# Kernel tuning notes

Hardware: AMD Instinct MI355X
Metric: run time of the kernel (lower is better)

## Reference

```python
import jax, jax.numpy as jnp
import numpy as np

B, S, D, H = 2, 2048, 1024, 16
HD = D // H  # head_dim = 64
INIT_STD = 0.02


def rotate_half(x):
    half = x.shape[-1] // 2
    return jnp.concatenate((-x[..., half:], x[..., :half]), axis=-1)


def setup_inputs() -> dict:
    key = jax.random.key(0)
    ks = jax.random.split(key, 6)
    inputs_q = jax.random.normal(ks[0], (B, S, D), dtype=jnp.float32)
    # causal mask, shape [B, 1, S, S] (broadcasts over heads)
    mask = jnp.broadcast_to(jnp.tril(jnp.ones((S, S), dtype=bool))[None, None], (B, 1, S, S))
    Wq = jax.random.normal(ks[1], (D, D), dtype=jnp.float32) * INIT_STD
    Wk = jax.random.normal(ks[2], (D, D), dtype=jnp.float32) * INIT_STD
    Wv = jax.random.normal(ks[3], (D, D), dtype=jnp.float32) * INIT_STD
    Wo = jax.random.normal(ks[4], (D, D), dtype=jnp.float32) * INIT_STD
    bq = jnp.zeros((D,), jnp.float32)
    bk = jnp.zeros((D,), jnp.float32)
    bv = jnp.zeros((D,), jnp.float32)
    bo = jnp.zeros((D,), jnp.float32)
    return {"inputs_q": inputs_q, "mask": mask, "Wq": Wq, "bq": bq, "Wk": Wk, "bk": bk,
            "Wv": Wv, "bv": bv, "Wo": Wo, "bo": bo}


def reference(inputs_q, mask, Wq, bq, Wk, bk, Wv, bv, Wo, bo):
    b, s, d = inputs_q.shape
    h, hd = H, d // H
    # QKV projections, split heads -> [b, s, h, hd]
    q = (inputs_q @ Wq + bq).reshape(b, s, h, hd)
    k = (inputs_q @ Wk + bk).reshape(b, s, h, hd)
    v = (inputs_q @ Wv + bv).reshape(b, s, h, hd)
    # rotary position embedding (GPT-J/Llama style: duplicated freqs over halves)
    pos = jnp.arange(s, dtype=jnp.float32)
    inv_freq = 1.0 / (10000.0 ** (jnp.arange(0, hd, 2, dtype=jnp.float32) / hd))
    freqs = pos[:, None] * inv_freq[None, :]              # [s, hd//2]
    emb = jnp.concatenate((freqs, freqs), axis=-1)        # [s, hd]
    sin = jnp.sin(emb)[None, :, None, :]                  # [1, s, 1, hd]
    cos = jnp.cos(emb)[None, :, None, :]
    q = q * cos + rotate_half(q) * sin
    k = k * cos + rotate_half(k) * sin
    # additive attention bias from boolean mask
    bias = jnp.where(mask, 0.0, jnp.finfo(jnp.float32).min)  # [b, 1, s, s]
    scores = jnp.einsum('bqhd,bkhd->bhqk', q, k) / jnp.sqrt(jnp.float32(hd)) + bias
    attn = jax.nn.softmax(scores, axis=-1)                   # [b, h, q, k]
    out = jnp.einsum('bhqk,bkhd->bqhd', attn, v).reshape(b, s, d)
    return out @ Wo + bo
```

## Files before the change

kernel.cpp:

```cpp
#include <hip/hip_runtime.h>
#include <math.h>

typedef unsigned short u16;
typedef unsigned int   u32;
typedef __attribute__((ext_vector_type(8))) short bf16x8;
typedef __attribute__((ext_vector_type(4))) short s16x4;
typedef __attribute__((ext_vector_type(4))) float f32x4;

#define BB 2
#define SS 2048
#define DD 1024
#define HH 16
#define HD 64
#define MM (BB*SS)
#define QKVN 3072

__device__ __forceinline__ u16 f2bf(float f) {
    u32 u = __float_as_uint(f);
    return (u16)((u + 0x7fffu + ((u >> 16) & 1u)) >> 16);
}
__device__ __forceinline__ float bf2f(u16 h) {
    return __uint_as_float(((u32)h) << 16);
}
__device__ __forceinline__ u32 cvt_pk_bf16(float lo, float hi) {
    u32 r;
    asm("v_cvt_pk_bf16_f32 %0, %1, %2" : "=v"(r) : "v"(lo), "v"(hi));
    return r;
}
__device__ __forceinline__ void gload16(const void* g, void* l) {
    __builtin_amdgcn_global_load_lds(
        (const __attribute__((address_space(1))) u32*)g,
        (__attribute__((address_space(3))) u32*)l, 16, 0, 0);
}

__global__ __launch_bounds__(256) void prep_kernel(
        const float* __restrict__ x,
        const float* __restrict__ W0, const float* __restrict__ W1,
        const float* __restrict__ W2, const float* __restrict__ W3,
        const float* __restrict__ b0, const float* __restrict__ b1,
        const float* __restrict__ b2,
        u16* __restrict__ Xb,
        u16* __restrict__ T0, u16* __restrict__ T1,
        u16* __restrict__ T2, u16* __restrict__ T3,
        float* __restrict__ bcat) {
    const int t = threadIdx.x;

    if (blockIdx.z == 4) {
        const int bid = blockIdx.y * 16 + blockIdx.x;
        #pragma unroll 4
        for (int it = 0; it < 16; ++it) {
            int i = (bid * 16 + it) * 256 + t;
            float4 v = reinterpret_cast<const float4*>(x)[i];
            u32 lo = (u32)f2bf(v.x) | ((u32)f2bf(v.y) << 16);
            u32 hi = (u32)f2bf(v.z) | ((u32)f2bf(v.w) << 16);
            reinterpret_cast<uint2*>(Xb)[i] = make_uint2(lo, hi);
        }
        if (bid < 12) {
            int i = bid * 256 + t;
            bcat[i] = (i < 1024) ? b0[i] : (i < 2048) ? b1[i - 1024] : b2[i - 2048];
        }
        return;
    }

    const float* W; u16* T;
    switch (blockIdx.z) {
        case 0:  W = W0; T = T0; break;
        case 1:  W = W1; T = T1; break;
        case 2:  W = W2; T = T2; break;
        default: W = W3; T = T3; break;
    }
    __shared__ float L[64][65];
    const int k0 = blockIdx.x * 64, n0 = blockIdx.y * 64;
    #pragma unroll
    for (int rep = 0; rep < 4; ++rep) {
        int row = rep * 16 + (t >> 4);
        int col = (t & 15) * 4;
        float4 v = *reinterpret_cast<const float4*>(&W[(size_t)(k0 + row) * DD + n0 + col]);
        L[row][col] = v.x; L[row][col+1] = v.y; L[row][col+2] = v.z; L[row][col+3] = v.w;
    }
    __syncthreads();
    #pragma unroll
    for (int rep = 0; rep < 2; ++rep) {
        int q  = t + rep * 256;
        int n  = q >> 3, sl = q & 7;
        u32 w[4];
        #pragma unroll
        for (int e = 0; e < 4; ++e) {
            float a = L[sl*8 + 2*e][n];
            float b = L[sl*8 + 2*e + 1][n];
            w[e] = (u32)f2bf(a) | ((u32)f2bf(b) << 16);
        }
        *reinterpret_cast<uint4*>(&T[(size_t)(n0 + n) * DD + k0 + sl*8]) =
            make_uint4(w[0], w[1], w[2], w[3]);
    }
}

template <typename OT, int BN, bool ROPE>
__global__ __launch_bounds__(256) void gemm_bf16(
        const u16* __restrict__ A, const u16* __restrict__ Bt,
        const float* __restrict__ bias, OT* __restrict__ C, int N) {
    constexpr int K = DD;
    constexpr int NJ = BN / 32;
    __shared__ __align__(16) u16 As[2][128 * 32];
    __shared__ __align__(16) u16 Bs[2][BN * 32];
    const int tid  = threadIdx.x;
    const int lane = tid & 63, w = tid >> 6;
    const int g = lane >> 4, c = lane & 15;
    const int wr = w >> 1, wc = w & 1;
    const int rowbase = blockIdx.x * 128;
    const int colbase = blockIdx.y * BN;

    auto stage = [&](int t, int bf) {
        const int k0 = t * 32;
        #pragma unroll
        for (int i = 0; i < 2; ++i) {
            int row = w * 32 + i * 16 + (lane >> 2);
            int sl  = lane & 3;
            gload16(&A [(size_t)(rowbase + row) * K + k0 + sl * 8],
                    &As[bf][(w * 32 + i * 16) * 32]);
        }
        #pragma unroll
        for (int i = 0; i < BN / 64; ++i) {
            int rb  = w * (BN / 4) + i * 16;
            int row = rb + (lane >> 2);
            int sl  = lane & 3;
            gload16(&Bt[(size_t)(colbase + row) * K + k0 + sl * 8],
                    &Bs[bf][rb * 32]);
        }
    };

    f32x4 acc[4][NJ];
    #pragma unroll
    for (int i = 0; i < 4; ++i)
        #pragma unroll
        for (int j = 0; j < NJ; ++j) acc[i][j] = (f32x4){0.f, 0.f, 0.f, 0.f};

    stage(0, 0);
    __syncthreads();

    for (int t = 0; t < K / 32; ++t) {
        const int cur = t & 1;
        if (t + 1 < K / 32) stage(t + 1, cur ^ 1);
        bf16x8 af[4], bfr[NJ];
        #pragma unroll
        for (int mi = 0; mi < 4; ++mi)
            af[mi] = *reinterpret_cast<const bf16x8*>(
                &As[cur][(wr * 64 + mi * 16 + c) * 32 + g * 8]);
        #pragma unroll
        for (int nj = 0; nj < NJ; ++nj)
            bfr[nj] = *reinterpret_cast<const bf16x8*>(
                &Bs[cur][(wc * (BN / 2) + nj * 16 + c) * 32 + g * 8]);
        #pragma unroll
        for (int mi = 0; mi < 4; ++mi)
            #pragma unroll
            for (int nj = 0; nj < NJ; ++nj)
                acc[mi][nj] = __builtin_amdgcn_mfma_f32_16x16x32_bf16(
                    af[mi], bfr[nj], acc[mi][nj], 0, 0, 0);
        __syncthreads();
    }

    if constexpr (ROPE) {
        const int region = colbase >> 10;
        const float invf0 = exp2f(-0.41524101186f * (float)c);
        const float invf1 = exp2f(-0.41524101186f * (float)(16 + c));
        #pragma unroll
        for (int mi = 0; mi < 4; ++mi)
            #pragma unroll
            for (int r = 0; r < 4; ++r) {
                const int rowg = rowbase + wr * 64 + mi * 16 + g * 4 + r;
                const float s = (float)(rowg & (SS - 1));
                #pragma unroll
                for (int nj = 0; nj < 2; ++nj) {
                    const int col_lo = colbase + wc * 64 + nj * 16 + c;
                    float lo = acc[mi][nj][r]     + bias[col_lo];
                    float hi = acc[mi][nj + 2][r] + bias[col_lo + 32];
                    if (region < 2) {
                        const float f = s * (nj ? invf1 : invf0);
                        float sn, cs;
                        __sincosf(f, &sn, &cs);
                        float rlo = lo * cs - hi * sn;
                        float rhi = hi * cs + lo * sn;
                        if (region == 0) { rlo *= 0.125f; rhi *= 0.125f; }
                        lo = rlo; hi = rhi;
                    }
                    C[(size_t)rowg * N + col_lo]      = (OT)f2bf(lo);
                    C[(size_t)rowg * N + col_lo + 32] = (OT)f2bf(hi);
                }
            }
    } else {
        #pragma unroll
        for (int mi = 0; mi < 4; ++mi)
            #pragma unroll
            for (int nj = 0; nj < NJ; ++nj) {
                int colg = colbase + wc * (BN / 2) + nj * 16 + c;
                float bv = bias[colg];
                #pragma unroll
                for (int r = 0; r < 4; ++r) {
                    int rowg = rowbase + wr * 64 + mi * 16 + g * 4 + r;
                    float v = acc[mi][nj][r] + bv;
                    if constexpr (sizeof(OT) == 2) C[(size_t)rowg * N + colg] = (OT)f2bf(v);
                    else                           C[(size_t)rowg * N + colg] = v;
                }
            }
    }
}

__global__ __launch_bounds__(512) void attn_mfma(
        const u16* __restrict__ qb, const u16* __restrict__ kb,
        const u16* __restrict__ vb, u16* __restrict__ ob) {
    const int bid = blockIdx.x;
    const int bh  = bid & 31;
    const int p   = bid >> 5;
    const int b   = bh >> 4, h = bh & 15;
    const int tid = threadIdx.x;
    const int lane = tid & 63, wq = tid >> 6;
    const int g = lane >> 4, c = lane & 15;

    __shared__ u16 Ks[3][64 * 64];
    __shared__ u16 Vt[3][64 * 66];

    const int krow = tid >> 3;
    const int ksl  = tid & 7;

    auto load_tile = [&](int kt, uint4& kr, uint4& vr) {
        const size_t base = (size_t)(b * SS + kt * 64 + krow) * QKVN + h * 64 + ksl * 8;
        kr = *reinterpret_cast<const uint4*>(&kb[base]);
        vr = *reinterpret_cast<const uint4*>(&vb[base]);
    };
    auto write_tile = [&](int bf, const uint4& kr, const uint4& vr) {
        *reinterpret_cast<uint4*>(&Ks[bf][krow * 64 + ((ksl ^ (krow & 7)) * 8)]) = kr;
        u32 ww[4] = {kr.x ^ kr.x ^ vr.x, vr.y, vr.z, vr.w};
        ww[0] = vr.x;
        #pragma unroll
        for (int e = 0; e < 4; ++e) {
            Vt[bf][(ksl * 8 + 2 * e    ) * 66 + krow] = (u16)(ww[e] & 0xffffu);
            Vt[bf][(ksl * 8 + 2 * e + 1) * 66 + krow] = (u16)(ww[e] >> 16);
        }
    };

    for (int half = 0; half < 2; ++half) {
        const int qt  = half ? p : (15 - p);
        const int qw0 = qt * 128 + wq * 16;
        const int nkt = qt * 2 + 2;

        bf16x8 qf[2];
        #pragma unroll
        for (int ks = 0; ks < 2; ++ks)
            qf[ks] = *reinterpret_cast<const bf16x8*>(
                &qb[(size_t)(b * SS + qw0 + c) * QKVN + h*64 + ks*32 + g*8]);

        f32x4 of[4];
        #pragma unroll
        for (int i = 0; i < 4; ++i) of[i] = (f32x4){0.f, 0.f, 0.f, 0.f};
        float mv = -1e30f;
        float lv = 0.f;

        uint4 kA, vA, kB, vB;

        auto body = [&](int kt, uint4& kW, uint4& vW, uint4& kL, uint4& vL) {
            const int cur = kt % 3;
            const int k0  = kt * 64;
            if (kt + 2 < nkt) load_tile(kt + 2, kL, vL);
            __syncthreads();

            if (k0 <= qw0 + 15) {
                f32x4 sf[4];
                #pragma unroll
                for (int i = 0; i < 4; ++i) sf[i] = (f32x4){0.f, 0.f, 0.f, 0.f};
                __builtin_amdgcn_s_setprio(1);
                #pragma unroll
                for (int ks = 0; ks < 2; ++ks)
                    #pragma unroll
                    for (int mi = 0; mi < 4; ++mi) {
                        int row = mi*16 + c;
                        bf16x8 kf = *reinterpret_cast<const bf16x8*>(
                            &Ks[cur][row*64 + (((ks*4 + g) ^ (row & 7)) * 8)]);
                        sf[mi] = __builtin_amdgcn_mfma_f32_16x16x32_bf16(
                            kf, qf[ks], sf[mi], 0, 0, 0);
                    }
                __builtin_amdgcn_s_setprio(0);

                if (k0 + 64 > qw0) {
                    const int qv = qw0 + c;
                    #pragma unroll
                    for (int mi = 0; mi < 4; ++mi) {
                        int key = k0 + mi*16 + g*4;
                        #pragma unroll
                        for (int r = 0; r < 4; ++r)
                            if (key + r > qv) sf[mi][r] = -1e30f;
                    }
                }

                float pmax = -1e30f;
                #pragma unroll
                for (int mi = 0; mi < 4; ++mi)
                    #pragma unroll
                    for (int r = 0; r < 4; ++r) pmax = fmaxf(pmax, sf[mi][r]);
                pmax = fmaxf(pmax, __shfl_xor(pmax, 16));
                pmax = fmaxf(pmax, __shfl_xor(pmax, 32));
                if (!__all(pmax - mv <= 8.0f)) {
                    float mnew = fmaxf(mv, pmax);
                    float corr = __expf(mv - mnew);
                    mv = mnew;
                    lv *= corr;
                    #pragma unroll
                    for (int mid = 0; mid < 4; ++mid) of[mid] *= corr;
                }
                float pp[4][4]; float ls = 0.f;
                #pragma unroll
                for (int mi = 0; mi < 4; ++mi)
                    #pragma unroll
                    for (int r = 0; r < 4; ++r) {
                        float e = __expf(sf[mi][r] - mv);
                        pp[mi][r] = e; ls += e;
                    }
                ls += __shfl_xor(ls, 16);
                ls += __shfl_xor(ls, 32);
                lv += ls;
                union PB { u32 u[4]; bf16x8 v; } pb[2];
                #pragma unroll
                for (int ks = 0; ks < 2; ++ks) {
                    pb[ks].u[0] = cvt_pk_bf16(pp[2*ks][0],     pp[2*ks][1]);
                    pb[ks].u[1] = cvt_pk_bf16(pp[2*ks][2],     pp[2*ks][3]);
                    pb[ks].u[2] = cvt_pk_bf16(pp[2*ks + 1][0], pp[2*ks + 1][1]);
                    pb[ks].u[3] = cvt_pk_bf16(pp[2*ks + 1][2], pp[2*ks + 1][3]);
                }

                __builtin_amdgcn_s_setprio(1);
                #pragma unroll
                for (int mid = 0; mid < 4; ++mid) {
                    int d = mid*16 + c;
                    #pragma unroll
                    for (int ks = 0; ks < 2; ++ks) {
                        union { s16x4 hh[2]; bf16x8 v; } vv;
                        vv.hh[0] = *reinterpret_cast<const s16x4*>(&Vt[cur][d*66 + ks*32 + 4*g]);
                        vv.hh[1] = *reinterpret_cast<const s16x4*>(&Vt[cur][d*66 + ks*32 + 16 + 4*g]);
                        of[mid] = __builtin_amdgcn_mfma_f32_16x16x32_bf16(
                            vv.v, pb[ks].v, of[mid], 0, 0, 0);
                    }
                }
                __builtin_amdgcn_s_setprio(0);
            }

            if (kt + 1 < nkt) write_tile((kt + 1) % 3, kW, vW);
        };

        load_tile(0, kB, vB);
        __syncthreads();
        write_tile(0, kB, vB);
        load_tile(1, kA, vA);

        for (int kt2 = 0; kt2 < nkt; kt2 += 2) {
            body(kt2,     kA, vA, kB, vB);
            body(kt2 + 1, kB, vB, kA, vA);
        }

        {
            float inv = 1.0f / lv;
            int qv = qw0 + c;
            #pragma unroll
            for (int mid = 0; mid < 4; ++mid) {
                u32 lo = cvt_pk_bf16(of[mid][0] * inv, of[mid][1] * inv);
                u32 hi = cvt_pk_bf16(of[mid][2] * inv, of[mid][3] * inv);
                *reinterpret_cast<uint2*>(
                    &ob[(size_t)(b * SS + qv) * DD + h*64 + mid*16 + g*4]) =
                    make_uint2(lo, hi);
            }
        }
    }
}

extern "C" void kernel_launch(void* const* d_in, const int* in_sizes, int n_in,
                              void* d_out, int out_size, void* d_ws, size_t ws_size,
                              hipStream_t stream) {
    const float* x  = (const float*)d_in[0];
    const float* Wq = (const float*)d_in[2];
    const float* bq = (const float*)d_in[3];
    const float* Wk = (const float*)d_in[4];
    const float* bk = (const float*)d_in[5];
    const float* Wv = (const float*)d_in[6];
    const float* bv = (const float*)d_in[7];
    const float* Wo = (const float*)d_in[8];
    const float* bo = (const float*)d_in[9];
    float* out = (float*)d_out;

    u16* Xb   = (u16*)d_ws;
    u16* Wcat = Xb   + (size_t)MM * DD;
    u16* Wot  = Wcat + (size_t)3 * DD * DD;
    u16* qkv  = Wot  + (size_t)DD * DD;
    u16* abuf = qkv  + (size_t)MM * QKVN;
    float* bcat = (float*)(abuf + (size_t)MM * DD);

    prep_kernel<<<dim3(16, 16, 5), 256, 0, stream>>>(
        x, Wq, Wk, Wv, Wo, bq, bk, bv,
        Xb, Wcat, Wcat + (size_t)DD * DD, Wcat + (size_t)2 * DD * DD, Wot, bcat);

    gemm_bf16<u16, 128, true><<<dim3(32, 24), 256, 0, stream>>>(Xb, Wcat, bcat, qkv, QKVN);

    attn_mfma<<<256, 512, 0, stream>>>(qkv, qkv + 1024, qkv + 2048, abuf);

    gemm_bf16<float, 64, false><<<dim3(32, 16), 256, 0, stream>>>(abuf, Wot, bo, out, DD);
}
```

Measured before the change: 121.5 us.

## Split attention KV tiles across wave pairs with 32-row query tiles and merge

```diff
diff --git a/kernel.cpp b/kernel.cpp
--- a/kernel.cpp
+++ b/kernel.cpp
@@ -215,9 +215,12 @@
     const int tid = threadIdx.x;
     const int lane = tid & 63, wq = tid >> 6;
     const int g = lane >> 4, c = lane & 15;
+    const int qg = wq >> 1;
+    const int kg = wq & 1;
 
     __shared__ u16 Ks[3][64 * 64];
     __shared__ u16 Vt[3][64 * 66];
+    __shared__ float Mrg[4][64][36];
 
     const int krow = tid >> 3;
     const int ksl  = tid & 7;
@@ -229,8 +232,7 @@
     };
     auto write_tile = [&](int bf, const uint4& kr, const uint4& vr) {
         *reinterpret_cast<uint4*>(&Ks[bf][krow * 64 + ((ksl ^ (krow & 7)) * 8)]) = kr;
-        u32 ww[4] = {kr.x ^ kr.x ^ vr.x, vr.y, vr.z, vr.w};
-        ww[0] = vr.x;
+        u32 ww[4] = {vr.x, vr.y, vr.z, vr.w};
         #pragma unroll
         for (int e = 0; e < 4; ++e) {
             Vt[bf][(ksl * 8 + 2 * e    ) * 66 + krow] = (u16)(ww[e] & 0xffffu);
@@ -240,20 +242,24 @@
 
     for (int half = 0; half < 2; ++half) {
         const int qt  = half ? p : (15 - p);
-        const int qw0 = qt * 128 + wq * 16;
+        const int qw0 = qt * 128 + qg * 32;
         const int nkt = qt * 2 + 2;
 
-        bf16x8 qf[2];
-        #pragma unroll
-        for (int ks = 0; ks < 2; ++ks)
-            qf[ks] = *reinterpret_cast<const bf16x8*>(
-                &qb[(size_t)(b * SS + qw0 + c) * QKVN + h*64 + ks*32 + g*8]);
-
-        f32x4 of[4];
-        #pragma unroll
-        for (int i = 0; i < 4; ++i) of[i] = (f32x4){0.f, 0.f, 0.f, 0.f};
-        float mv = -1e30f;
-        float lv = 0.f;
+        bf16x8 qf[2][2];
+        #pragma unroll
+        for (int nj = 0; nj < 2; ++nj)
+            #pragma unroll
+            for (int ks = 0; ks < 2; ++ks)
+                qf[nj][ks] = *reinterpret_cast<const bf16x8*>(
+                    &qb[(size_t)(b * SS + qw0 + nj*16 + c) * QKVN + h*64 + ks*32 + g*8]);
+
+        f32x4 of[4][2];
+        #pragma unroll
+        for (int i = 0; i < 4; ++i)
+            #pragma unroll
+            for (int j = 0; j < 2; ++j) of[i][j] = (f32x4){0.f, 0.f, 0.f, 0.f};
+        float mv[2] = {-1e30f, -1e30f};
+        float lv[2] = {0.f, 0.f};
 
         uint4 kA, vA, kB, vB;
 
@@ -263,10 +269,12 @@
             if (kt + 2 < nkt) load_tile(kt + 2, kL, vL);
             __syncthreads();
 
-            if (k0 <= qw0 + 15) {
-                f32x4 sf[4];
-                #pragma unroll
-                for (int i = 0; i < 4; ++i) sf[i] = (f32x4){0.f, 0.f, 0.f, 0.f};
+            if (((kt ^ kg) & 1) == 0 && k0 <= qw0 + 31) {
+                f32x4 sf[4][2];
+                #pragma unroll
+                for (int i = 0; i < 4; ++i)
+                    #pragma unroll
+                    for (int j = 0; j < 2; ++j) sf[i][j] = (f32x4){0.f, 0.f, 0.f, 0.f};
                 __builtin_amdgcn_s_setprio(1);
                 #pragma unroll
                 for (int ks = 0; ks < 2; ++ks)
@@ -275,55 +283,63 @@
                         int row = mi*16 + c;
                         bf16x8 kf = *reinterpret_cast<const bf16x8*>(
                             &Ks[cur][row*64 + (((ks*4 + g) ^ (row & 7)) * 8)]);
-                        sf[mi] = __builtin_amdgcn_mfma_f32_16x16x32_bf16(
-                            kf, qf[ks], sf[mi], 0, 0, 0);
+                        #pragma unroll
+                        for (int nj = 0; nj < 2; ++nj)
+                            sf[mi][nj] = __builtin_amdgcn_mfma_f32_16x16x32_bf16(
+                                kf, qf[nj][ks], sf[mi][nj], 0, 0, 0);
                     }
                 __builtin_amdgcn_s_setprio(0);
 
                 if (k0 + 64 > qw0) {
-                    const int qv = qw0 + c;
                     #pragma unroll
                     for (int mi = 0; mi < 4; ++mi) {
                         int key = k0 + mi*16 + g*4;
                         #pragma unroll
-                        for (int r = 0; r < 4; ++r)
-                            if (key + r > qv) sf[mi][r] = -1e30f;
-                    }
-                }
-
-                float pmax = -1e30f;
-                #pragma unroll
-                for (int mi = 0; mi < 4; ++mi)
-                    #pragma unroll
-                    for (int r = 0; r < 4; ++r) pmax = fmaxf(pmax, sf[mi][r]);
-                pmax = fmaxf(pmax, __shfl_xor(pmax, 16));
-                pmax = fmaxf(pmax, __shfl_xor(pmax, 32));
-                if (!__all(pmax - mv <= 8.0f)) {
-                    float mnew = fmaxf(mv, pmax);
-                    float corr = __expf(mv - mnew);
-                    mv = mnew;
-                    lv *= corr;
-                    #pragma unroll
-                    for (int mid = 0; mid < 4; ++mid) of[mid] *= corr;
-                }
-                float pp[4][4]; float ls = 0.f;
-                #pragma unroll
-                for (int mi = 0; mi < 4; ++mi)
-                    #pragma unroll
-                    for (int r = 0; r < 4; ++r) {
-                        float e = __expf(sf[mi][r] - mv);
-                        pp[mi][r] = e; ls += e;
-                    }
-                ls += __shfl_xor(ls, 16);
-                ls += __shfl_xor(ls, 32);
-                lv += ls;
-                union PB { u32 u[4]; bf16x8 v; } pb[2];
-                #pragma unroll
-                for (int ks = 0; ks < 2; ++ks) {
-                    pb[ks].u[0] = cvt_pk_bf16(pp[2*ks][0],     pp[2*ks][1]);
-                    pb[ks].u[1] = cvt_pk_bf16(pp[2*ks][2],     pp[2*ks][3]);
-                    pb[ks].u[2] = cvt_pk_bf16(pp[2*ks + 1][0], pp[2*ks + 1][1]);
-                    pb[ks].u[3] = cvt_pk_bf16(pp[2*ks + 1][2], pp[2*ks + 1][3]);
+                        for (int nj = 0; nj < 2; ++nj) {
+                            int qv = qw0 + nj*16 + c;
+                            #pragma unroll
+                            for (int r = 0; r < 4; ++r)
+                                if (key + r > qv) sf[mi][nj][r] = -1e30f;
+                        }
+                    }
+                }
+
+                union PB { u32 u[4]; bf16x8 v; } pb[2][2];
+                #pragma unroll
+                for (int nj = 0; nj < 2; ++nj) {
+                    float pmax = -1e30f;
+                    #pragma unroll
+                    for (int mi = 0; mi < 4; ++mi)
+                        #pragma unroll
+                        for (int r = 0; r < 4; ++r) pmax = fmaxf(pmax, sf[mi][nj][r]);
+                    pmax = fmaxf(pmax, __shfl_xor(pmax, 16));
+                    pmax = fmaxf(pmax, __shfl_xor(pmax, 32));
+                    if (!__all(pmax - mv[nj] <= 8.0f)) {
+                        float mnew = fmaxf(mv[nj], pmax);
+                        float corr = __expf(mv[nj] - mnew);
+                        mv[nj] = mnew;
+                        lv[nj] *= corr;
+                        #pragma unroll
+                        for (int mid = 0; mid < 4; ++mid) of[mid][nj] *= corr;
+                    }
+                    float pp[4][4]; float ls = 0.f;
+                    #pragma unroll
+                    for (int mi = 0; mi < 4; ++mi)
+                        #pragma unroll
+                        for (int r = 0; r < 4; ++r) {
+                            float e = __expf(sf[mi][nj][r] - mv[nj]);
+                            pp[mi][r] = e; ls += e;
+                        }
+                    ls += __shfl_xor(ls, 16);
+                    ls += __shfl_xor(ls, 32);
+                    lv[nj] += ls;
+                    #pragma unroll
+                    for (int ks = 0; ks < 2; ++ks) {
+                        pb[nj][ks].u[0] = cvt_pk_bf16(pp[2*ks][0],     pp[2*ks][1]);
+                        pb[nj][ks].u[1] = cvt_pk_bf16(pp[2*ks][2],     pp[2*ks][3]);
+                        pb[nj][ks].u[2] = cvt_pk_bf16(pp[2*ks + 1][0], pp[2*ks + 1][1]);
+                        pb[nj][ks].u[3] = cvt_pk_bf16(pp[2*ks + 1][2], pp[2*ks + 1][3]);
+                    }
                 }
 
                 __builtin_amdgcn_s_setprio(1);
@@ -335,8 +351,10 @@
                         union { s16x4 hh[2]; bf16x8 v; } vv;
                         vv.hh[0] = *reinterpret_cast<const s16x4*>(&Vt[cur][d*66 + ks*32 + 4*g]);
                         vv.hh[1] = *reinterpret_cast<const s16x4*>(&Vt[cur][d*66 + ks*32 + 16 + 4*g]);
-                        of[mid] = __builtin_amdgcn_mfma_f32_16x16x32_bf16(
-                            vv.v, pb[ks].v, of[mid], 0, 0, 0);
+                        #pragma unroll
+                        for (int nj = 0; nj < 2; ++nj)
+                            of[mid][nj] = __builtin_amdgcn_mfma_f32_16x16x32_bf16(
+                                vv.v, pb[nj][ks].v, of[mid][nj], 0, 0, 0);
                     }
                 }
                 __builtin_amdgcn_s_setprio(0);
@@ -355,16 +373,39 @@
             body(kt2 + 1, kB, vB, kA, vA);
         }
 
-        {
-            float inv = 1.0f / lv;
-            int qv = qw0 + c;
-            #pragma unroll
-            for (int mid = 0; mid < 4; ++mid) {
-                u32 lo = cvt_pk_bf16(of[mid][0] * inv, of[mid][1] * inv);
-                u32 hi = cvt_pk_bf16(of[mid][2] * inv, of[mid][3] * inv);
-                *reinterpret_cast<uint2*>(
-                    &ob[(size_t)(b * SS + qv) * DD + h*64 + mid*16 + g*4]) =
-                    make_uint2(lo, hi);
+        if (kg == 1) {
+            float* m = &Mrg[qg][lane][0];
+            m[0] = mv[0]; m[1] = mv[1]; m[2] = lv[0]; m[3] = lv[1];
+            #pragma unroll
+            for (int mid = 0; mid < 4; ++mid)
+                #pragma unroll
+                for (int nj = 0; nj < 2; ++nj)
+                    #pragma unroll
+                    for (int r = 0; r < 4; ++r)
+                        m[4 + mid*8 + nj*4 + r] = of[mid][nj][r];
+        }
+        __syncthreads();
+        if (kg == 0) {
+            const float* m1 = &Mrg[qg][lane][0];
+            #pragma unroll
+            for (int nj = 0; nj < 2; ++nj) {
+                float mB = m1[nj];
+                float mm = fmaxf(mv[nj], mB);
+                float c0 = __expf(mv[nj] - mm);
+                float c1 = __expf(mB - mm);
+                float ll = lv[nj] * c0 + m1[2 + nj] * c1;
+                float inv = 1.0f / ll;
+                int qv = qw0 + nj*16 + c;
+                #pragma unroll
+                for (int mid = 0; mid < 4; ++mid) {
+                    float o0 = (of[mid][nj][0]*c0 + m1[4 + mid*8 + nj*4 + 0]*c1) * inv;
+                    float o1 = (of[mid][nj][1]*c0 + m1[4 + mid*8 + nj*4 + 1]*c1) * inv;
+                    float o2 = (of[mid][nj][2]*c0 + m1[4 + mid*8 + nj*4 + 2]*c1) * inv;
+                    float o3 = (of[mid][nj][3]*c0 + m1[4 + mid*8 + nj*4 + 3]*c1) * inv;
+                    *reinterpret_cast<uint2*>(
+                        &ob[(size_t)(b * SS + qv) * DD + h*64 + mid*16 + g*4]) =
+                        make_uint2(cvt_pk_bf16(o0, o1), cvt_pk_bf16(o2, o3));
+                }
             }
         }
     }
```

After: 139.3 us. 14.7% more time.

## Process two KV tiles per barrier with double-buffered tile pairs in attention

Applied to the files above, without the earlier changes.

```diff
diff --git a/kernel.cpp b/kernel.cpp
--- a/kernel.cpp
+++ b/kernel.cpp
@@ -216,8 +216,8 @@
     const int lane = tid & 63, wq = tid >> 6;
     const int g = lane >> 4, c = lane & 15;
 
-    __shared__ u16 Ks[3][64 * 64];
-    __shared__ u16 Vt[3][64 * 66];
+    __shared__ u16 Ks[2][2][64 * 64];
+    __shared__ u16 Vt[2][2][64 * 66];
 
     const int krow = tid >> 3;
     const int ksl  = tid & 7;
@@ -227,14 +227,13 @@
         kr = *reinterpret_cast<const uint4*>(&kb[base]);
         vr = *reinterpret_cast<const uint4*>(&vb[base]);
     };
-    auto write_tile = [&](int bf, const uint4& kr, const uint4& vr) {
-        *reinterpret_cast<uint4*>(&Ks[bf][krow * 64 + ((ksl ^ (krow & 7)) * 8)]) = kr;
-        u32 ww[4] = {kr.x ^ kr.x ^ vr.x, vr.y, vr.z, vr.w};
-        ww[0] = vr.x;
+    auto write_tile = [&](int pb, int s, const uint4& kr, const uint4& vr) {
+        *reinterpret_cast<uint4*>(&Ks[pb][s][krow * 64 + ((ksl ^ (krow & 7)) * 8)]) = kr;
+        u32 ww[4] = {vr.x, vr.y, vr.z, vr.w};
         #pragma unroll
         for (int e = 0; e < 4; ++e) {
-            Vt[bf][(ksl * 8 + 2 * e    ) * 66 + krow] = (u16)(ww[e] & 0xffffu);
-            Vt[bf][(ksl * 8 + 2 * e + 1) * 66 + krow] = (u16)(ww[e] >> 16);
+            Vt[pb][s][(ksl * 8 + 2 * e    ) * 66 + krow] = (u16)(ww[e] & 0xffffu);
+            Vt[pb][s][(ksl * 8 + 2 * e + 1) * 66 + krow] = (u16)(ww[e] >> 16);
         }
     };
 
@@ -255,105 +254,120 @@
         float mv = -1e30f;
         float lv = 0.f;
 
-        uint4 kA, vA, kB, vB;
-
-        auto body = [&](int kt, uint4& kW, uint4& vW, uint4& kL, uint4& vL) {
-            const int cur = kt % 3;
-            const int k0  = kt * 64;
-            if (kt + 2 < nkt) load_tile(kt + 2, kL, vL);
+        auto compute_tile = [&](int kt, int pbuf, int slot) {
+            const int k0 = kt * 64;
+            f32x4 sf[4];
+            #pragma unroll
+            for (int i = 0; i < 4; ++i) sf[i] = (f32x4){0.f, 0.f, 0.f, 0.f};
+            __builtin_amdgcn_s_setprio(1);
+            #pragma unroll
+            for (int ks = 0; ks < 2; ++ks)
+                #pragma unroll
+                for (int mi = 0; mi < 4; ++mi) {
+                    int row = mi*16 + c;
+                    bf16x8 kf = *reinterpret_cast<const bf16x8*>(
+                        &Ks[pbuf][slot][row*64 + (((ks*4 + g) ^ (row & 7)) * 8)]);
+                    sf[mi] = __builtin_amdgcn_mfma_f32_16x16x32_bf16(
+                        kf, qf[ks], sf[mi], 0, 0, 0);
+                }
+            __builtin_amdgcn_s_setprio(0);
+
+            if (k0 + 64 > qw0) {
+                const int qv = qw0 + c;
+                #pragma unroll
+                for (int mi = 0; mi < 4; ++mi) {
+                    int key = k0 + mi*16 + g*4;
+                    #pragma unroll
+                    for (int r = 0; r < 4; ++r)
+                        if (key + r > qv) sf[mi][r] = -1e30f;
+                }
+            }
+
+            float pmax = -1e30f;
+            #pragma unroll
+            for (int mi = 0; mi < 4; ++mi)
+                #pragma unroll
+                for (int r = 0; r < 4; ++r) pmax = fmaxf(pmax, sf[mi][r]);
+            pmax = fmaxf(pmax, __shfl_xor(pmax, 16));
+            pmax = fmaxf(pmax, __shfl_xor(pmax, 32));
+            if (!__all(pmax - mv <= 8.0f)) {
+                float mnew = fmaxf(mv, pmax);
+                float corr = __expf(mv - mnew);
+                mv = mnew;
+                lv *= corr;
+                #pragma unroll
+                for (int mid = 0; mid < 4; ++mid) of[mid] *= corr;
+            }
+            float pp[4][4]; float ls = 0.f;
+            #pragma unroll
+            for (int mi = 0; mi < 4; ++mi)
+                #pragma unroll
+                for (int r = 0; r < 4; ++r) {
+                    float e = __expf(sf[mi][r] - mv);
+                    pp[mi][r] = e; ls += e;
+                }
+            ls += __shfl_xor(ls, 16);
+            ls += __shfl_xor(ls, 32);
+            lv += ls;
+            union PB { u32 u[4]; bf16x8 v; } pb2[2];
+            #pragma unroll
+            for (int ks = 0; ks < 2; ++ks) {
+                pb2[ks].u[0] = cvt_pk_bf16(pp[2*ks][0],     pp[2*ks][1]);
+                pb2[ks].u[1] = cvt_pk_bf16(pp[2*ks][2],     pp[2*ks][3]);
+                pb2[ks].u[2] = cvt_pk_bf16(pp[2*ks + 1][0], pp[2*ks + 1][1]);
+                pb2[ks].u[3] = cvt_pk_bf16(pp[2*ks + 1][2], pp[2*ks + 1][3]);
+            }
+
+            __builtin_amdgcn_s_setprio(1);
+            #pragma unroll
+            for (int mid = 0; mid < 4; ++mid) {
+                int d = mid*16 + c;
+                #pragma unroll
+                for (int ks = 0; ks < 2; ++ks) {
+                    union { s16x4 hh[2]; bf16x8 v; } vv;
+                    vv.hh[0] = *reinterpret_cast<const s16x4*>(&Vt[pbuf][slot][d*66 + ks*32 + 4*g]);
+                    vv.hh[1] = *reinterpret_cast<const s16x4*>(&Vt[pbuf][slot][d*66 + ks*32 + 16 + 4*g]);
+                    of[mid] = __builtin_amdgcn_mfma_f32_16x16x32_bf16(
+                        vv.v, pb2[ks].v, of[mid], 0, 0, 0);
+                }
+            }
+            __builtin_amdgcn_s_setprio(0);
+        };
+
+        uint4 k0A, v0A, k1A, v1A, k0B, v0B, k1B, v1B;
+
+        auto phase = [&](int ph,
+                         uint4& kW0, uint4& vW0, uint4& kW1, uint4& vW1,
+                         uint4& kL0, uint4& vL0, uint4& kL1, uint4& vL1) {
+            const int cur = ph & 1;
+            const int t0 = ph * 2;
+            if (t0 + 4 < nkt) {
+                load_tile(t0 + 4, kL0, vL0);
+                load_tile(t0 + 5, kL1, vL1);
+            }
             __syncthreads();
-
-            if (k0 <= qw0 + 15) {
-                f32x4 sf[4];
-                #pragma unroll
-                for (int i = 0; i < 4; ++i) sf[i] = (f32x4){0.f, 0.f, 0.f, 0.f};
-                __builtin_amdgcn_s_setprio(1);
-                #pragma unroll
-                for (int ks = 0; ks < 2; ++ks)
-                    #pragma unroll
-                    for (int mi = 0; mi < 4; ++mi) {
-                        int row = mi*16 + c;
-                        bf16x8 kf = *reinterpret_cast<const bf16x8*>(
-                            &Ks[cur][row*64 + (((ks*4 + g) ^ (row & 7)) * 8)]);
-                        sf[mi] = __builtin_amdgcn_mfma_f32_16x16x32_bf16(
-                            kf, qf[ks], sf[mi], 0, 0, 0);
-                    }
-                __builtin_amdgcn_s_setprio(0);
-
-                if (k0 + 64 > qw0) {
-                    const int qv = qw0 + c;
-                    #pragma unroll
-                    for (int mi = 0; mi < 4; ++mi) {
-                        int key = k0 + mi*16 + g*4;
-                        #pragma unroll
-                        for (int r = 0; r < 4; ++r)
-                            if (key + r > qv) sf[mi][r] = -1e30f;
-                    }
-                }
-
-                float pmax = -1e30f;
-                #pragma unroll
-                for (int mi = 0; mi < 4; ++mi)
-                    #pragma unroll
-                    for (int r = 0; r < 4; ++r) pmax = fmaxf(pmax, sf[mi][r]);
-                pmax = fmaxf(pmax, __shfl_xor(pmax, 16));
-                pmax = fmaxf(pmax, __shfl_xor(pmax, 32));
-                if (!__all(pmax - mv <= 8.0f)) {
-                    float mnew = fmaxf(mv, pmax);
-                    float corr = __expf(mv - mnew);
-                    mv = mnew;
-                    lv *= corr;
-                    #pragma unroll
-                    for (int mid = 0; mid < 4; ++mid) of[mid] *= corr;
-                }
-                float pp[4][4]; float ls = 0.f;
-                #pragma unroll
-                for (int mi = 0; mi < 4; ++mi)
-                    #pragma unroll
-                    for (int r = 0; r < 4; ++r) {
-                        float e = __expf(sf[mi][r] - mv);
-                        pp[mi][r] = e; ls += e;
-                    }
-                ls += __shfl_xor(ls, 16);
-                ls += __shfl_xor(ls, 32);
-                lv += ls;
-                union PB { u32 u[4]; bf16x8 v; } pb[2];
-                #pragma unroll
-                for (int ks = 0; ks < 2; ++ks) {
-                    pb[ks].u[0] = cvt_pk_bf16(pp[2*ks][0],     pp[2*ks][1]);
-                    pb[ks].u[1] = cvt_pk_bf16(pp[2*ks][2],     pp[2*ks][3]);
-                    pb[ks].u[2] = cvt_pk_bf16(pp[2*ks + 1][0], pp[2*ks + 1][1]);
-                    pb[ks].u[3] = cvt_pk_bf16(pp[2*ks + 1][2], pp[2*ks + 1][3]);
-                }
-
-                __builtin_amdgcn_s_setprio(1);
-                #pragma unroll
-                for (int mid = 0; mid < 4; ++mid) {
-                    int d = mid*16 + c;
-                    #pragma unroll
-                    for (int ks = 0; ks < 2; ++ks) {
-                        union { s16x4 hh[2]; bf16x8 v; } vv;
-                        vv.hh[0] = *reinterpret_cast<const s16x4*>(&Vt[cur][d*66 + ks*32 + 4*g]);
-                        vv.hh[1] = *reinterpret_cast<const s16x4*>(&Vt[cur][d*66 + ks*32 + 16 + 4*g]);
-                        of[mid] = __builtin_amdgcn_mfma_f32_16x16x32_bf16(
-                            vv.v, pb[ks].v, of[mid], 0, 0, 0);
-                    }
-                }
-                __builtin_amdgcn_s_setprio(0);
-            }
-
-            if (kt + 1 < nkt) write_tile((kt + 1) % 3, kW, vW);
+            if (t0 * 64 <= qw0 + 15)       compute_tile(t0,     cur, 0);
+            if ((t0 + 1) * 64 <= qw0 + 15) compute_tile(t0 + 1, cur, 1);
+            if (t0 + 2 < nkt) {
+                write_tile(cur ^ 1, 0, kW0, vW0);
+                write_tile(cur ^ 1, 1, kW1, vW1);
+            }
         };
 
-        load_tile(0, kB, vB);
+        load_tile(0, k0A, v0A);
+        load_tile(1, k1A, v1A);
         __syncthreads();
-        write_tile(0, kB, vB);
-        load_tile(1, kA, vA);
-
-        for (int kt2 = 0; kt2 < nkt; kt2 += 2) {
-            body(kt2,     kA, vA, kB, vB);
-            body(kt2 + 1, kB, vB, kA, vA);
-        }
+        write_tile(0, 0, k0A, v0A);
+        write_tile(0, 1, k1A, v1A);
+        if (2 < nkt) { load_tile(2, k0B, v0B); load_tile(3, k1B, v1B); }
+
+        const int nph = nkt >> 1;
+        for (int ph = 0; ph + 1 < nph; ph += 2) {
+            phase(ph,     k0B, v0B, k1B, v1B, k0A, v0A, k1A, v1A);
+            phase(ph + 1, k0A, v0A, k1A, v1A, k0B, v0B, k1B, v1B);
+        }
+        if (nph & 1)
+            phase(nph - 1, k0B, v0B, k1B, v1B, k0A, v0A, k1A, v1A);
 
         {
             float inv = 1.0f / lv;
```

Measured after the change: 118.7 us. -2.3%, faster.
